# Performance work log

Hardware: AMD Instinct MI355X
Metric: run time of the kernel (lower is better)

Reference implementation:

```python
import jax, jax.numpy as jnp
import numpy as np

N, H, C, G = 50000, 16, 8, 128   # nodes, heads, per-head channels, graphs
F_IN, NUM_CLASSES = 128, 2
E = 800000
HC = H * C
NEG_SLOPE = 0.2
BN_EPS = 1e-5


def setup_inputs() -> dict:
    key = jax.random.key(0)
    ks = jax.random.split(key, 32)
    s = 0.1
    p = lambda k, shape: (jax.random.normal(k, shape, jnp.float32) * s)
    inp = {
        "x": jax.random.normal(ks[0], (N, F_IN), jnp.float32),
        "edge_index": jax.random.randint(ks[1], (2, E), 0, N, dtype=jnp.int32),
        "batch": jnp.sort(jax.random.randint(ks[2], (N,), 0, G, dtype=jnp.int32)),
        # GAT layer 1 (in=F_IN)
        "W1": p(ks[3], (F_IN, HC)), "b1": p(ks[4], (HC,)),
        "asrc1": p(ks[5], (H, C)), "adst1": p(ks[6], (H, C)),
        "g1": 1.0 + p(ks[7], (HC,)), "beta1": p(ks[8], (HC,)),
        # GAT layer 2 (in=HC)
        "W2": p(ks[9], (HC, HC)), "b2": p(ks[10], (HC,)),
        "asrc2": p(ks[11], (H, C)), "adst2": p(ks[12], (H, C)),
        "g2": 1.0 + p(ks[13], (HC,)), "beta2": p(ks[14], (HC,)),
        # GAT layer 3
        "W3": p(ks[15], (HC, HC)), "b3": p(ks[16], (HC,)),
        "asrc3": p(ks[17], (H, C)), "adst3": p(ks[18], (H, C)),
        "g3": 1.0 + p(ks[19], (HC,)), "beta3": p(ks[20], (HC,)),
        # final linear + bn4
        "Wl": p(ks[21], (2 * HC, NUM_CLASSES)), "bl": p(ks[22], (NUM_CLASSES,)),
        "g4": 1.0 + p(ks[23], (NUM_CLASSES,)), "beta4": p(ks[24], (NUM_CLASSES,)),
    }
    return inp


def _gat(x, src, dst, W, b, asrc, adst):
    # x: [N, F_in] -> h: [N, H, C]
    h = (x @ W).reshape(N, H, C)
    a_s = jnp.einsum("nhc,hc->nh", h, asrc)  # [N,H]
    a_d = jnp.einsum("nhc,hc->nh", h, adst)
    e = jax.nn.leaky_relu(a_s[src] + a_d[dst], NEG_SLOPE)  # [E',H]
    # per-destination softmax (every node has a self loop -> segments non-empty)
    e_max = jax.ops.segment_max(e, dst, num_segments=N)
    ex = jnp.exp(e - e_max[dst])
    denom = jax.ops.segment_sum(ex, dst, num_segments=N)
    alpha = ex / (denom[dst] + 1e-16)  # [E',H]
    out = jax.ops.segment_sum(h[src] * alpha[:, :, None], dst, num_segments=N)
    return out.reshape(N, HC) + b


def _bn(x, g, beta):
    mu = jnp.mean(x, axis=0)
    var = jnp.mean((x - mu) ** 2, axis=0)  # biased, training-mode BN
    return (x - mu) * jax.lax.rsqrt(var + BN_EPS) * g + beta


def reference(x, edge_index, batch,
              W1, b1, asrc1, adst1, g1, beta1,
              W2, b2, asrc2, adst2, g2, beta2,
              W3, b3, asrc3, adst3, g3, beta3,
              Wl, bl, g4, beta4):
    # add self loops once (add_self_loops=True in every GATConv)
    loop = jnp.arange(N, dtype=edge_index.dtype)
    src = jnp.concatenate([edge_index[0], loop])
    dst = jnp.concatenate([edge_index[1], loop])

    h = jax.nn.relu(_bn(_gat(x, src, dst, W1, b1, asrc1, adst1), g1, beta1))
    h = jax.nn.relu(_bn(_gat(h, src, dst, W2, b2, asrc2, adst2), g2, beta2))
    h = jax.nn.relu(_bn(_gat(h, src, dst, W3, b3, asrc3, adst3), g3, beta3))

    pooled_sum = jax.ops.segment_sum(h, batch, num_segments=G)        # [G,HC]
    cnt = jax.ops.segment_sum(jnp.ones((N,), h.dtype), batch, num_segments=G)
    pooled_mean = pooled_sum / jnp.maximum(cnt, 1.0)[:, None]
    z = jnp.concatenate([pooled_mean, pooled_sum], axis=1)            # [G,2*HC]
    z = z @ Wl + bl
    return _bn(z, g4, beta4)
```

## Files before the change

### kernel.cpp

```cpp
#include <hip/hip_runtime.h>

#define NN 50000
#define NHEADS 16
#define NGRAPH 128
#define NEDGE 800000
#define NEP (NEDGE + NN)

#define EPB 2048
#define NBLK 416
#define NBUK 391
#define CASTB 3125
#define WTB 192

typedef float4 f4;
typedef __attribute__((ext_vector_type(4))) float f32x4;
typedef __attribute__((ext_vector_type(8))) short s8;

__device__ inline unsigned short f2b(float f) {
  union { float f; unsigned u; } v; v.f = f;
  unsigned r = v.u + 0x7FFFu + ((v.u >> 16) & 1u);
  return (unsigned short)(r >> 16);
}
__device__ inline float b2f(unsigned u16) {
  union { unsigned u; float f; } v; v.u = u16 << 16;
  return v.f;
}


__global__ __launch_bounds__(256) void k_bhist(const int* __restrict__ ei, int* __restrict__ cntmat) {
  __shared__ int hist[NBUK];
  int t = threadIdx.x, b = blockIdx.x;
  for (int k = t; k < NBUK; k += 256) hist[k] = 0;
  __syncthreads();
  int i0 = b * EPB;
  int i1 = i0 + EPB < NEP ? i0 + EPB : NEP;
  for (int i = i0 + t; i < i1; i += 256) {
    int d = (i < NEDGE) ? ei[NEDGE + i] : (i - NEDGE);
    atomicAdd(&hist[d >> 7], 1);
  }
  __syncthreads();
  for (int k = t; k < NBUK; k += 256) cntmat[b * NBUK + k] = hist[k];
}

__global__ __launch_bounds__(512) void k_bscan(int* __restrict__ cntmat, int* __restrict__ btotal) {
  __shared__ int buf[512];
  int t = threadIdx.x, k = blockIdx.x;
  int v = (t < NBLK) ? cntmat[t * NBUK + k] : 0;
  buf[t] = v;
  __syncthreads();
  for (int off = 1; off < 512; off <<= 1) {
    int y = (t >= off) ? buf[t - off] : 0;
    __syncthreads();
    buf[t] += y;
    __syncthreads();
  }
  if (t < NBLK) cntmat[t * NBUK + k] = buf[t] - v;
  if (t == 511) btotal[k] = buf[511];
}

__global__ __launch_bounds__(512) void k_bbase(const int* __restrict__ btotal, int* __restrict__ bbase) {
  __shared__ int buf[512];
  int t = threadIdx.x;
  int v = (t < NBUK) ? btotal[t] : 0;
  buf[t] = v;
  __syncthreads();
  for (int off = 1; off < 512; off <<= 1) {
    int y = (t >= off) ? buf[t - off] : 0;
    __syncthreads();
    buf[t] += y;
    __syncthreads();
  }
  if (t < NBUK) bbase[t] = buf[t] - v;
  if (t == 511) bbase[NBUK] = buf[511];
}

__global__ __launch_bounds__(256) void k_bscatter(const int* __restrict__ ei, const int* __restrict__ cntmat,
                                                  const int* __restrict__ bbase, unsigned* __restrict__ pairs) {
  __shared__ int cur[NBUK];
  int t = threadIdx.x, b = blockIdx.x;
  for (int k = t; k < NBUK; k += 256) cur[k] = bbase[k] + cntmat[b * NBUK + k];
  __syncthreads();
  int i0 = b * EPB;
  int i1 = i0 + EPB < NEP ? i0 + EPB : NEP;
  for (int i = i0 + t; i < i1; i += 256) {
    int s, d;
    if (i < NEDGE) { s = ei[i]; d = ei[NEDGE + i]; }
    else { s = d = i - NEDGE; }
    int pos = atomicAdd(&cur[d >> 7], 1);
    pairs[pos] = ((unsigned)(d & 127) << 16) | (unsigned)s;
  }
}

__global__ __launch_bounds__(256) void k_bfinal(const unsigned* __restrict__ pairs, const int* __restrict__ bbase,
                                                int* __restrict__ row_off, int* __restrict__ colp) {
  __shared__ int cnt[128];
  __shared__ int buf[128];
  __shared__ int cur[128];
  int t = threadIdx.x, k = blockIdx.x;
  int n0 = k << 7;
  if (t < 128) cnt[t] = 0;
  __syncthreads();
  int p0 = bbase[k], p1 = bbase[k + 1];
  for (int i = p0 + t; i < p1; i += 256) atomicAdd(&cnt[pairs[i] >> 16], 1);
  __syncthreads();
  if (t < 128) buf[t] = cnt[t];
  __syncthreads();
  for (int off = 1; off < 128; off <<= 1) {
    int y = (t < 128 && t >= off) ? buf[t - off] : 0;
    __syncthreads();
    if (t < 128) buf[t] += y;
    __syncthreads();
  }
  if (t < 128) {
    int excl = buf[t] - cnt[t];
    cur[t] = p0 + excl;
    if (n0 + t < NN) row_off[n0 + t] = p0 + excl;
  }
  if (k == NBUK - 1 && t == 0) row_off[NN] = p1;
  __syncthreads();
  for (int i = p0 + t; i < p1; i += 256) {
    unsigned r = pairs[i];
    int pos = atomicAdd(&cur[r >> 16], 1);
    colp[pos] = (int)(r & 0xffffu);
  }
}


__global__ __launch_bounds__(256) void k_prep(const float* __restrict__ X, unsigned short* __restrict__ Xb,
                                              const float* __restrict__ W0, const float* __restrict__ W1, const float* __restrict__ W2,
                                              unsigned short* __restrict__ T0, unsigned short* __restrict__ T1, unsigned short* __restrict__ T2,
                                              const int* __restrict__ batch, int* __restrict__ gstart) {
  int b = blockIdx.x, t = threadIdx.x;
  if (b < CASTB) {
    int i = b * 256 + t;
    const f4* X4 = (const f4*)X;
    f4 a = X4[2 * i], c = X4[2 * i + 1];
    uint4 o;
    o.x = (unsigned)f2b(a.x) | ((unsigned)f2b(a.y) << 16);
    o.y = (unsigned)f2b(a.z) | ((unsigned)f2b(a.w) << 16);
    o.z = (unsigned)f2b(c.x) | ((unsigned)f2b(c.y) << 16);
    o.w = (unsigned)f2b(c.z) | ((unsigned)f2b(c.w) << 16);
    ((uint4*)Xb)[i] = o;
  } else if (b < CASTB + WTB) {
    int idx = (b - CASTB) * 256 + t;
    int L = idx >> 14, r = idx & 16383;
    int n = r >> 7, kk = r & 127;
    const float* W = (L == 0) ? W0 : (L == 1) ? W1 : W2;
    unsigned short* T = (L == 0) ? T0 : (L == 1) ? T1 : T2;
    T[n * 128 + kk] = f2b(W[kk * 128 + n]);
  } else {
    int g = t;
    if (g > NGRAPH) return;
    int lo = 0, hi = NN;
    while (lo < hi) { int mid = (lo + hi) >> 1; if (batch[mid] < g) lo = mid + 1; else hi = mid; }
    gstart[g] = lo;
  }
}


__global__ __launch_bounds__(256) void k_gemm(const unsigned short* __restrict__ Xb, const unsigned short* __restrict__ Wt,
                                              unsigned short* __restrict__ Hb) {
  int w = threadIdx.x >> 6, l = threadIdx.x & 63;
  int r0 = blockIdx.x * 128 + w * 32;
  int lr = l & 15, lg = l >> 4;
  f32x4 acc[2][8];
#pragma unroll
  for (int m = 0; m < 2; ++m)
#pragma unroll
    for (int n = 0; n < 8; ++n) acc[m][n] = (f32x4){0.f, 0.f, 0.f, 0.f};

#pragma unroll
  for (int ks = 0; ks < 4; ++ks) {
    int koff = ks * 32 + lg * 8;
    s8 a[2];
#pragma unroll
    for (int m = 0; m < 2; ++m) {
      int row = r0 + m * 16 + lr;
      row = (row < NN) ? row : (NN - 1);
      a[m] = *(const s8*)(Xb + (size_t)row * 128 + koff);
    }
    s8 b[8];
#pragma unroll
    for (int n = 0; n < 8; ++n)
      b[n] = *(const s8*)(Wt + (size_t)(n * 16 + lr) * 128 + koff);
#pragma unroll
    for (int m = 0; m < 2; ++m)
#pragma unroll
      for (int n = 0; n < 8; ++n)
        acc[m][n] = __builtin_amdgcn_mfma_f32_16x16x32_bf16(a[m], b[n], acc[m][n], 0, 0, 0);
  }

#pragma unroll
  for (int m = 0; m < 2; ++m) {
    int rowb = r0 + m * 16 + lg * 4;
#pragma unroll
    for (int n = 0; n < 8; ++n) {
      int colb = n * 16 + lr;
#pragma unroll
      for (int reg = 0; reg < 4; ++reg) {
        int row = rowb + reg;
        if (row < NN) Hb[(size_t)row * 128 + colb] = f2b(acc[m][n][reg]);
      }
    }
  }
}


__global__ __launch_bounds__(256) void k_coef(const unsigned short* __restrict__ Hb, const float* __restrict__ asrc,
                                              const float* __restrict__ adst, unsigned short* __restrict__ Asb, float* __restrict__ Ad) {
  int idx = blockIdx.x * 256 + threadIdx.x;
  if (idx >= NN * NHEADS) return;
  int n = idx >> 4, hd = idx & 15;
  uint4 hv = *(const uint4*)(Hb + (size_t)n * 128 + hd * 8);
  float h0 = b2f(hv.x & 0xffff), h1 = b2f(hv.x >> 16);
  float h2 = b2f(hv.y & 0xffff), h3 = b2f(hv.y >> 16);
  float h4 = b2f(hv.z & 0xffff), h5 = b2f(hv.z >> 16);
  float h6 = b2f(hv.w & 0xffff), h7 = b2f(hv.w >> 16);
  const f4* s4 = (const f4*)(asrc + hd * 8);
  const f4* d4 = (const f4*)(adst + hd * 8);
  f4 sa = s4[0], sb = s4[1], da = d4[0], db = d4[1];
  float as_v = h0 * sa.x + h1 * sa.y + h2 * sa.z + h3 * sa.w + h4 * sb.x + h5 * sb.y + h6 * sb.z + h7 * sb.w;
  float ad_v = h0 * da.x + h1 * da.y + h2 * da.z + h3 * da.w + h4 * db.x + h5 * db.y + h6 * db.z + h7 * db.w;
  Asb[idx] = f2b(as_v);
  Ad[idx] = ad_v;
}


__global__ __launch_bounds__(256) void k_agg(const unsigned short* __restrict__ Hb, const unsigned short* __restrict__ Asb,
                                             const float* __restrict__ Ad,
                                             const int* __restrict__ row_off, const int* __restrict__ col,
                                             unsigned short* __restrict__ Vb) {
  int node = blockIdx.x * 8 + (threadIdx.x >> 5);
  int l = threadIdx.x & 31;
  int h = l & 15, par = l >> 4;
  int e0 = row_off[node], e1 = row_off[node + 1];
  float adh = Ad[node * 16 + h];
  float den = 0.f;
  float acc[8] = {0.f, 0.f, 0.f, 0.f, 0.f, 0.f, 0.f, 0.f};
  int j = e0 + par;
  for (; j + 14 < e1; j += 16) {
    int s[8];
#pragma unroll
    for (int q = 0; q < 8; ++q) s[q] = col[j + 2 * q];
    float a[8];
#pragma unroll
    for (int q = 0; q < 8; ++q) a[q] = b2f(Asb[s[q] * 16 + h]);
    uint4 p[8];
#pragma unroll
    for (int q = 0; q < 8; ++q) p[q] = *(const uint4*)(Hb + (size_t)s[q] * 128 + h * 8);
#pragma unroll
    for (int q = 0; q < 8; ++q) {
      float e = a[q] + adh;
      e = (e > 0.f) ? e : 0.2f * e;
      a[q] = __expf(e);
      den += a[q];
    }
#pragma unroll
    for (int q = 0; q < 8; ++q) {
      acc[0] += a[q] * b2f(p[q].x & 0xffff); acc[1] += a[q] * b2f(p[q].x >> 16);
      acc[2] += a[q] * b2f(p[q].y & 0xffff); acc[3] += a[q] * b2f(p[q].y >> 16);
      acc[4] += a[q] * b2f(p[q].z & 0xffff); acc[5] += a[q] * b2f(p[q].z >> 16);
      acc[6] += a[q] * b2f(p[q].w & 0xffff); acc[7] += a[q] * b2f(p[q].w >> 16);
    }
  }
  for (; j + 6 < e1; j += 8) {
    int s[4];
#pragma unroll
    for (int q = 0; q < 4; ++q) s[q] = col[j + 2 * q];
    float a[4];
#pragma unroll
    for (int q = 0; q < 4; ++q) a[q] = b2f(Asb[s[q] * 16 + h]);
    uint4 p[4];
#pragma unroll
    for (int q = 0; q < 4; ++q) p[q] = *(const uint4*)(Hb + (size_t)s[q] * 128 + h * 8);
#pragma unroll
    for (int q = 0; q < 4; ++q) {
      float e = a[q] + adh;
      e = (e > 0.f) ? e : 0.2f * e;
      a[q] = __expf(e);
      den += a[q];
    }
#pragma unroll
    for (int q = 0; q < 4; ++q) {
      acc[0] += a[q] * b2f(p[q].x & 0xffff); acc[1] += a[q] * b2f(p[q].x >> 16);
      acc[2] += a[q] * b2f(p[q].y & 0xffff); acc[3] += a[q] * b2f(p[q].y >> 16);
      acc[4] += a[q] * b2f(p[q].z & 0xffff); acc[5] += a[q] * b2f(p[q].z >> 16);
      acc[6] += a[q] * b2f(p[q].w & 0xffff); acc[7] += a[q] * b2f(p[q].w >> 16);
    }
  }
  for (; j < e1; j += 2) {
    int s0 = col[j];
    float a0 = b2f(Asb[s0 * 16 + h]) + adh;
    uint4 p0 = *(const uint4*)(Hb + (size_t)s0 * 128 + h * 8);
    a0 = (a0 > 0.f) ? a0 : 0.2f * a0;
    float x0 = __expf(a0);
    den += x0;
    acc[0] += x0 * b2f(p0.x & 0xffff);
    acc[1] += x0 * b2f(p0.x >> 16);
    acc[2] += x0 * b2f(p0.y & 0xffff);
    acc[3] += x0 * b2f(p0.y >> 16);
    acc[4] += x0 * b2f(p0.z & 0xffff);
    acc[5] += x0 * b2f(p0.z >> 16);
    acc[6] += x0 * b2f(p0.w & 0xffff);
    acc[7] += x0 * b2f(p0.w >> 16);
  }
  den += __shfl_xor(den, 16);
#pragma unroll
  for (int k = 0; k < 8; ++k) acc[k] += __shfl_xor(acc[k], 16);
  if (par == 0) {
    float inv = 1.f / (den + 1e-16f);
    uint4 o;
    o.x = (unsigned)f2b(acc[0] * inv) | ((unsigned)f2b(acc[1] * inv) << 16);
    o.y = (unsigned)f2b(acc[2] * inv) | ((unsigned)f2b(acc[3] * inv) << 16);
    o.z = (unsigned)f2b(acc[4] * inv) | ((unsigned)f2b(acc[5] * inv) << 16);
    o.w = (unsigned)f2b(acc[6] * inv) | ((unsigned)f2b(acc[7] * inv) << 16);
    *(uint4*)(Vb + (size_t)node * 128 + h * 8) = o;
  }
}


#define BN_CHUNK 391

__global__ __launch_bounds__(256) void k_bnreduce(const unsigned short* __restrict__ Vb, float* __restrict__ partS, float* __restrict__ partQ) {
  int t = threadIdx.x;
  int c4 = t & 31, rs = t >> 5;
  int r0 = blockIdx.x * BN_CHUNK + rs;
  int rend = blockIdx.x * BN_CHUNK + BN_CHUNK;
  if (rend > NN) rend = NN;
  float s0 = 0.f, s1 = 0.f, s2 = 0.f, s3 = 0.f;
  float q0 = 0.f, q1 = 0.f, q2 = 0.f, q3 = 0.f;
  for (int r = r0; r < rend; r += 8) {
    uint2 p = *(const uint2*)(Vb + (size_t)r * 128 + c4 * 4);
    float v0 = b2f(p.x & 0xffff), v1 = b2f(p.x >> 16);
    float v2 = b2f(p.y & 0xffff), v3 = b2f(p.y >> 16);
    s0 += v0; s1 += v1; s2 += v2; s3 += v3;
    q0 += v0 * v0; q1 += v1 * v1; q2 += v2 * v2; q3 += v3 * v3;
  }
  __shared__ float sm[8][32][8];
  sm[rs][c4][0] = s0; sm[rs][c4][1] = s1; sm[rs][c4][2] = s2; sm[rs][c4][3] = s3;
  sm[rs][c4][4] = q0; sm[rs][c4][5] = q1; sm[rs][c4][6] = q2; sm[rs][c4][7] = q3;
  __syncthreads();
  if (t < 32) {
#pragma unroll
    for (int k = 0; k < 4; ++k) {
      float S = 0.f, Q = 0.f;
#pragma unroll
      for (int r = 0; r < 8; ++r) { S += sm[r][t][k]; Q += sm[r][t][4 + k]; }
      partS[blockIdx.x * 128 + t * 4 + k] = S;
      partQ[blockIdx.x * 128 + t * 4 + k] = Q;
    }
  }
}

__global__ __launch_bounds__(512) void k_bnfin(const float* __restrict__ partS, const float* __restrict__ partQ,
                                               const float* __restrict__ gam, const float* __restrict__ bet,
                                               float* __restrict__ sc) {
  int t = threadIdx.x;
  int c = t & 127, q = (t >> 7) & 1, hf = t >> 8;
  const float* src = q ? partQ : partS;
  float s = 0.f;
#pragma unroll 8
  for (int i = hf * 64; i < hf * 64 + 64; ++i) s += src[i * 128 + c];
  __shared__ float sm[512];
  sm[t] = s;
  __syncthreads();
  if (t < 128) {
    float S = sm[t] + sm[t + 256];
    float Q = sm[t + 128] + sm[t + 384];
    float mean = S * (1.f / NN);
    float var = fmaxf(Q * (1.f / NN) - mean * mean, 0.f);
    float sg = gam[t] * rsqrtf(var + 1e-5f);
    sc[t] = sg;
    sc[128 + t] = bet[t] - mean * sg;
  }
}

__global__ __launch_bounds__(256) void k_bnapply(const unsigned short* __restrict__ Vb, unsigned short* __restrict__ Xb,
                                                 const float* __restrict__ sc) {
  int idx = blockIdx.x * 256 + threadIdx.x;
  int c4 = idx & 31;
  uint2 p = ((const uint2*)Vb)[idx];
  f4 s = ((const f4*)sc)[c4], sh = ((const f4*)sc)[32 + c4];
  float v0 = fmaxf(b2f(p.x & 0xffff) * s.x + sh.x, 0.f);
  float v1 = fmaxf(b2f(p.x >> 16)    * s.y + sh.y, 0.f);
  float v2 = fmaxf(b2f(p.y & 0xffff) * s.z + sh.z, 0.f);
  float v3 = fmaxf(b2f(p.y >> 16)    * s.w + sh.w, 0.f);
  uint2 o;
  o.x = (unsigned)f2b(v0) | ((unsigned)f2b(v1) << 16);
  o.y = (unsigned)f2b(v2) | ((unsigned)f2b(v3) << 16);
  ((uint2*)Xb)[idx] = o;
}


__global__ __launch_bounds__(256) void k_pool(const unsigned short* __restrict__ Vb, const int* __restrict__ gstart,
                                              float* __restrict__ pooled) {
  int g = blockIdx.x >> 2, chunk = blockIdx.x & 3;
  int t = threadIdx.x;
  int c4 = t & 31, rs = t >> 5;
  int r0 = gstart[g], r1 = gstart[g + 1];
  float s0 = 0.f, s1 = 0.f, s2 = 0.f, s3 = 0.f;
  for (int r = r0 + chunk + 4 * rs; r < r1; r += 32) {
    uint2 p = *(const uint2*)(Vb + (size_t)r * 128 + c4 * 4);
    s0 += b2f(p.x & 0xffff); s1 += b2f(p.x >> 16);
    s2 += b2f(p.y & 0xffff); s3 += b2f(p.y >> 16);
  }
  __shared__ float sm[8][32][4];
  sm[rs][c4][0] = s0; sm[rs][c4][1] = s1; sm[rs][c4][2] = s2; sm[rs][c4][3] = s3;
  __syncthreads();
  if (t < 32) {
#pragma unroll
    for (int k = 0; k < 4; ++k) {
      float S = 0.f;
#pragma unroll
      for (int r = 0; r < 8; ++r) S += sm[r][t][k];
      atomicAdd(&pooled[g * 128 + t * 4 + k], S);
    }
  }
}

__global__ __launch_bounds__(256) void k_final(const float* __restrict__ pooled, const int* __restrict__ gstart,
                                               const float* __restrict__ Wl, const float* __restrict__ bl,
                                               const float* __restrict__ g4, const float* __restrict__ b4,
                                               float* __restrict__ out) {
  int t = threadIdx.x;
  int g = t >> 1, cls = t & 1;
  float cnt = fmaxf((float)(gstart[g + 1] - gstart[g]), 1.f);
  float inv = 1.f / cnt;
  float z = bl[cls];
  for (int f = 0; f < 128; ++f) {
    float ps = pooled[g * 128 + f];
    z += ps * inv * Wl[f * 2 + cls] + ps * Wl[(128 + f) * 2 + cls];
  }
  __shared__ float zs[256];
  __shared__ float st[4];
  zs[t] = z;
  __syncthreads();
  if (t < 2) {
    float s = 0.f, s2 = 0.f;
    for (int gg = 0; gg < 128; ++gg) { float v = zs[gg * 2 + t]; s += v; s2 += v * v; }
    float mean = s * (1.f / 128.f);
    float var = s2 * (1.f / 128.f) - mean * mean;
    var = fmaxf(var, 0.f);
    float sc = g4[t] * rsqrtf(var + 1e-5f);
    st[t] = sc; st[2 + t] = b4[t] - mean * sc;
  }
  __syncthreads();
  out[t] = zs[t] * st[cls] + st[2 + cls];
}


extern "C" void kernel_launch(void* const* d_in, const int* in_sizes, int n_in,
                              void* d_out, int out_size, void* d_ws, size_t ws_size,
                              hipStream_t stream) {
  const float* x     = (const float*)d_in[0];
  const int*   ei    = (const int*)d_in[1];
  const int*   batch = (const int*)d_in[2];
  const float* W[3]    = {(const float*)d_in[3],  (const float*)d_in[9],  (const float*)d_in[15]};
  const float* asrc[3] = {(const float*)d_in[5],  (const float*)d_in[11], (const float*)d_in[17]};
  const float* adst[3] = {(const float*)d_in[6],  (const float*)d_in[12], (const float*)d_in[18]};
  const float* gam[3]  = {(const float*)d_in[7],  (const float*)d_in[13], (const float*)d_in[19]};
  const float* bet[3]  = {(const float*)d_in[8],  (const float*)d_in[14], (const float*)d_in[20]};
  const float* Wl    = (const float*)d_in[21];
  const float* bl    = (const float*)d_in[22];
  const float* g4    = (const float*)d_in[23];
  const float* beta4 = (const float*)d_in[24];

  char* ws = (char*)d_ws;
  size_t off = 0;
  auto alloc = [&](size_t bytes) -> void* {
    void* p = (void*)(ws + off);
    off += (bytes + 255) & ~(size_t)255;
    return p;
  };

  int* row_off  = (int*)alloc((size_t)(NN + 1) * 4);
  int* col      = (int*)alloc((size_t)NEP * 4);
  int* cntmat   = (int*)alloc((size_t)NBLK * NBUK * 4);
  int* btotal   = (int*)alloc((size_t)NBUK * 4);
  int* bbase    = (int*)alloc((size_t)(NBUK + 1) * 4);
  unsigned* pairs = (unsigned*)alloc((size_t)NEP * 4);
  unsigned short* Xb = (unsigned short*)alloc((size_t)NN * 128 * 2);
  unsigned short* Hb = (unsigned short*)alloc((size_t)NN * 128 * 2);
  unsigned short* Vb = (unsigned short*)alloc((size_t)NN * 128 * 2);
  unsigned short* Asb = (unsigned short*)alloc((size_t)NN * 16 * 2);
  float* Ad     = (float*)alloc((size_t)NN * 16 * 4);
  unsigned short* Wt0 = (unsigned short*)alloc(16384 * 2);
  unsigned short* Wt1 = (unsigned short*)alloc(16384 * 2);
  unsigned short* Wt2 = (unsigned short*)alloc(16384 * 2);
  const unsigned short* Wt[3] = {Wt0, Wt1, Wt2};
  float* partS  = (float*)alloc(128 * 128 * 4);
  float* partQ  = (float*)alloc(128 * 128 * 4);
  float* bn_sc  = (float*)alloc(256 * 4);
  float* pooled = (float*)alloc((size_t)NGRAPH * 128 * 4);
  int* gstart   = (int*)alloc((size_t)(NGRAPH + 1) * 4);

  k_bhist<<<NBLK, 256, 0, stream>>>(ei, cntmat);
  k_bscan<<<NBUK, 512, 0, stream>>>(cntmat, btotal);
  k_bbase<<<1, 512, 0, stream>>>(btotal, bbase);
  k_bscatter<<<NBLK, 256, 0, stream>>>(ei, cntmat, bbase, pairs);
  k_bfinal<<<NBUK, 256, 0, stream>>>(pairs, bbase, row_off, col);

  k_prep<<<CASTB + WTB + 1, 256, 0, stream>>>(x, Xb, W[0], W[1], W[2], Wt0, Wt1, Wt2, batch, gstart);

  hipMemsetAsync(pooled, 0, (size_t)NGRAPH * 128 * 4, stream);

  for (int L = 0; L < 3; ++L) {
    k_gemm<<<(NN + 127) / 128, 256, 0, stream>>>(Xb, Wt[L], Hb);
    k_coef<<<(NN * 16) / 256, 256, 0, stream>>>(Hb, asrc[L], adst[L], Asb, Ad);
    k_agg<<<NN / 8, 256, 0, stream>>>(Hb, Asb, Ad, row_off, col, Vb);
    k_bnreduce<<<128, 256, 0, stream>>>(Vb, partS, partQ);
    k_bnfin<<<1, 512, 0, stream>>>(partS, partQ, gam[L], bet[L], bn_sc);
    k_bnapply<<<(NN * 32) / 256, 256, 0, stream>>>(Vb, Xb, bn_sc);
  }

  k_pool<<<NGRAPH * 4, 256, 0, stream>>>(Xb, gstart, pooled);
  k_final<<<1, 256, 0, stream>>>(pooled, gstart, Wl, bl, g4, beta4, (float*)d_out);
}
```

Baseline: 311.1 us.

## Fuse BN apply and ReLU into next GEMM's A-load and into pooling

Removes the standalone BN-apply kernel. The scale/shift plus ReLU now runs while the next layer's GEMM loads its A operand from Vb, and while pooling reads the final layer. This saves one full read and write of the node feature matrix per layer and one launch per layer. It also adds cheaper bf16 unpack helpers (masking instead of shifting for the high half) and an occupancy hint of 4 on k_agg. The cost is extra ALU work inside the GEMM load path.

```diff
diff --git a/kernel.cpp b/kernel.cpp
--- a/kernel.cpp
+++ b/kernel.cpp
@@ -23,6 +23,14 @@
 }
 __device__ inline float b2f(unsigned u16) {
   union { unsigned u; float f; } v; v.u = u16 << 16;
+  return v.f;
+}
+__device__ inline float blo(unsigned u) {
+  union { unsigned u; float f; } v; v.u = u << 16;
+  return v.f;
+}
+__device__ inline float bhi(unsigned u) {
+  union { unsigned u; float f; } v; v.u = u & 0xffff0000u;
   return v.f;
 }
 
@@ -158,8 +166,9 @@
 }
 
 
-__global__ __launch_bounds__(256) void k_gemm(const unsigned short* __restrict__ Xb, const unsigned short* __restrict__ Wt,
-                                              unsigned short* __restrict__ Hb) {
+template<int FUSE>
+__global__ __launch_bounds__(256) void k_gemm_t(const unsigned short* __restrict__ A, const unsigned short* __restrict__ Wt,
+                                                const float* __restrict__ sc, unsigned short* __restrict__ Hb) {
   int w = threadIdx.x >> 6, l = threadIdx.x & 63;
   int r0 = blockIdx.x * 128 + w * 32;
   int lr = l & 15, lg = l >> 4;
@@ -173,11 +182,36 @@
   for (int ks = 0; ks < 4; ++ks) {
     int koff = ks * 32 + lg * 8;
     s8 a[2];
-#pragma unroll
-    for (int m = 0; m < 2; ++m) {
-      int row = r0 + m * 16 + lr;
-      row = (row < NN) ? row : (NN - 1);
-      a[m] = *(const s8*)(Xb + (size_t)row * 128 + koff);
+    if constexpr (FUSE) {
+      f4 s0 = *(const f4*)(sc + koff),       s1 = *(const f4*)(sc + koff + 4);
+      f4 h0 = *(const f4*)(sc + 128 + koff), h1 = *(const f4*)(sc + 128 + koff + 4);
+#pragma unroll
+      for (int m = 0; m < 2; ++m) {
+        int row = r0 + m * 16 + lr;
+        row = (row < NN) ? row : (NN - 1);
+        uint4 raw = *(const uint4*)(A + (size_t)row * 128 + koff);
+        float v0 = fmaxf(blo(raw.x) * s0.x + h0.x, 0.f);
+        float v1 = fmaxf(bhi(raw.x) * s0.y + h0.y, 0.f);
+        float v2 = fmaxf(blo(raw.y) * s0.z + h0.z, 0.f);
+        float v3 = fmaxf(bhi(raw.y) * s0.w + h0.w, 0.f);
+        float v4 = fmaxf(blo(raw.z) * s1.x + h1.x, 0.f);
+        float v5 = fmaxf(bhi(raw.z) * s1.y + h1.y, 0.f);
+        float v6 = fmaxf(blo(raw.w) * s1.z + h1.z, 0.f);
+        float v7 = fmaxf(bhi(raw.w) * s1.w + h1.w, 0.f);
+        union { s8 v; uint4 u; } pk;
+        pk.u.x = (unsigned)f2b(v0) | ((unsigned)f2b(v1) << 16);
+        pk.u.y = (unsigned)f2b(v2) | ((unsigned)f2b(v3) << 16);
+        pk.u.z = (unsigned)f2b(v4) | ((unsigned)f2b(v5) << 16);
+        pk.u.w = (unsigned)f2b(v6) | ((unsigned)f2b(v7) << 16);
+        a[m] = pk.v;
+      }
+    } else {
+#pragma unroll
+      for (int m = 0; m < 2; ++m) {
+        int row = r0 + m * 16 + lr;
+        row = (row < NN) ? row : (NN - 1);
+        a[m] = *(const s8*)(A + (size_t)row * 128 + koff);
+      }
     }
     s8 b[8];
 #pragma unroll
@@ -212,10 +246,10 @@
   if (idx >= NN * NHEADS) return;
   int n = idx >> 4, hd = idx & 15;
   uint4 hv = *(const uint4*)(Hb + (size_t)n * 128 + hd * 8);
-  float h0 = b2f(hv.x & 0xffff), h1 = b2f(hv.x >> 16);
-  float h2 = b2f(hv.y & 0xffff), h3 = b2f(hv.y >> 16);
-  float h4 = b2f(hv.z & 0xffff), h5 = b2f(hv.z >> 16);
-  float h6 = b2f(hv.w & 0xffff), h7 = b2f(hv.w >> 16);
+  float h0 = blo(hv.x), h1 = bhi(hv.x);
+  float h2 = blo(hv.y), h3 = bhi(hv.y);
+  float h4 = blo(hv.z), h5 = bhi(hv.z);
+  float h6 = blo(hv.w), h7 = bhi(hv.w);
   const f4* s4 = (const f4*)(asrc + hd * 8);
   const f4* d4 = (const f4*)(adst + hd * 8);
   f4 sa = s4[0], sb = s4[1], da = d4[0], db = d4[1];
@@ -226,10 +260,10 @@
 }
 
 
-__global__ __launch_bounds__(256) void k_agg(const unsigned short* __restrict__ Hb, const unsigned short* __restrict__ Asb,
-                                             const float* __restrict__ Ad,
-                                             const int* __restrict__ row_off, const int* __restrict__ col,
-                                             unsigned short* __restrict__ Vb) {
+__global__ __launch_bounds__(256, 4) void k_agg(const unsigned short* __restrict__ Hb, const unsigned short* __restrict__ Asb,
+                                                const float* __restrict__ Ad,
+                                                const int* __restrict__ row_off, const int* __restrict__ col,
+                                                unsigned short* __restrict__ Vb) {
   int node = blockIdx.x * 8 + (threadIdx.x >> 5);
   int l = threadIdx.x & 31;
   int h = l & 15, par = l >> 4;
@@ -257,10 +291,10 @@
     }
 #pragma unroll
     for (int q = 0; q < 8; ++q) {
-      acc[0] += a[q] * b2f(p[q].x & 0xffff); acc[1] += a[q] * b2f(p[q].x >> 16);
-      acc[2] += a[q] * b2f(p[q].y & 0xffff); acc[3] += a[q] * b2f(p[q].y >> 16);
-      acc[4] += a[q] * b2f(p[q].z & 0xffff); acc[5] += a[q] * b2f(p[q].z >> 16);
-      acc[6] += a[q] * b2f(p[q].w & 0xffff); acc[7] += a[q] * b2f(p[q].w >> 16);
+      acc[0] += a[q] * blo(p[q].x); acc[1] += a[q] * bhi(p[q].x);
+      acc[2] += a[q] * blo(p[q].y); acc[3] += a[q] * bhi(p[q].y);
+      acc[4] += a[q] * blo(p[q].z); acc[5] += a[q] * bhi(p[q].z);
+      acc[6] += a[q] * blo(p[q].w); acc[7] += a[q] * bhi(p[q].w);
     }
   }
   for (; j + 6 < e1; j += 8) {
@@ -282,10 +316,10 @@
     }
 #pragma unroll
     for (int q = 0; q < 4; ++q) {
-      acc[0] += a[q] * b2f(p[q].x & 0xffff); acc[1] += a[q] * b2f(p[q].x >> 16);
-      acc[2] += a[q] * b2f(p[q].y & 0xffff); acc[3] += a[q] * b2f(p[q].y >> 16);
-      acc[4] += a[q] * b2f(p[q].z & 0xffff); acc[5] += a[q] * b2f(p[q].z >> 16);
-      acc[6] += a[q] * b2f(p[q].w & 0xffff); acc[7] += a[q] * b2f(p[q].w >> 16);
+      acc[0] += a[q] * blo(p[q].x); acc[1] += a[q] * bhi(p[q].x);
+      acc[2] += a[q] * blo(p[q].y); acc[3] += a[q] * bhi(p[q].y);
+      acc[4] += a[q] * blo(p[q].z); acc[5] += a[q] * bhi(p[q].z);
+      acc[6] += a[q] * blo(p[q].w); acc[7] += a[q] * bhi(p[q].w);
     }
   }
   for (; j < e1; j += 2) {
@@ -295,14 +329,10 @@
     a0 = (a0 > 0.f) ? a0 : 0.2f * a0;
     float x0 = __expf(a0);
     den += x0;
-    acc[0] += x0 * b2f(p0.x & 0xffff);
-    acc[1] += x0 * b2f(p0.x >> 16);
-    acc[2] += x0 * b2f(p0.y & 0xffff);
-    acc[3] += x0 * b2f(p0.y >> 16);
-    acc[4] += x0 * b2f(p0.z & 0xffff);
-    acc[5] += x0 * b2f(p0.z >> 16);
-    acc[6] += x0 * b2f(p0.w & 0xffff);
-    acc[7] += x0 * b2f(p0.w >> 16);
+    acc[0] += x0 * blo(p0.x); acc[1] += x0 * bhi(p0.x);
+    acc[2] += x0 * blo(p0.y); acc[3] += x0 * bhi(p0.y);
+    acc[4] += x0 * blo(p0.z); acc[5] += x0 * bhi(p0.z);
+    acc[6] += x0 * blo(p0.w); acc[7] += x0 * bhi(p0.w);
   }
   den += __shfl_xor(den, 16);
 #pragma unroll
@@ -331,8 +361,8 @@
   float q0 = 0.f, q1 = 0.f, q2 = 0.f, q3 = 0.f;
   for (int r = r0; r < rend; r += 8) {
     uint2 p = *(const uint2*)(Vb + (size_t)r * 128 + c4 * 4);
-    float v0 = b2f(p.x & 0xffff), v1 = b2f(p.x >> 16);
-    float v2 = b2f(p.y & 0xffff), v3 = b2f(p.y >> 16);
+    float v0 = blo(p.x), v1 = bhi(p.x);
+    float v2 = blo(p.y), v3 = bhi(p.y);
     s0 += v0; s1 += v1; s2 += v2; s3 += v3;
     q0 += v0 * v0; q1 += v1 * v1; q2 += v2 * v2; q3 += v3 * v3;
   }
@@ -375,34 +405,21 @@
   }
 }
 
-__global__ __launch_bounds__(256) void k_bnapply(const unsigned short* __restrict__ Vb, unsigned short* __restrict__ Xb,
-                                                 const float* __restrict__ sc) {
-  int idx = blockIdx.x * 256 + threadIdx.x;
-  int c4 = idx & 31;
-  uint2 p = ((const uint2*)Vb)[idx];
-  f4 s = ((const f4*)sc)[c4], sh = ((const f4*)sc)[32 + c4];
-  float v0 = fmaxf(b2f(p.x & 0xffff) * s.x + sh.x, 0.f);
-  float v1 = fmaxf(b2f(p.x >> 16)    * s.y + sh.y, 0.f);
-  float v2 = fmaxf(b2f(p.y & 0xffff) * s.z + sh.z, 0.f);
-  float v3 = fmaxf(b2f(p.y >> 16)    * s.w + sh.w, 0.f);
-  uint2 o;
-  o.x = (unsigned)f2b(v0) | ((unsigned)f2b(v1) << 16);
-  o.y = (unsigned)f2b(v2) | ((unsigned)f2b(v3) << 16);
-  ((uint2*)Xb)[idx] = o;
-}
-
-
-__global__ __launch_bounds__(256) void k_pool(const unsigned short* __restrict__ Vb, const int* __restrict__ gstart,
-                                              float* __restrict__ pooled) {
+
+__global__ __launch_bounds__(256) void k_pool(const unsigned short* __restrict__ Vb, const float* __restrict__ sc,
+                                              const int* __restrict__ gstart, float* __restrict__ pooled) {
   int g = blockIdx.x >> 2, chunk = blockIdx.x & 3;
   int t = threadIdx.x;
   int c4 = t & 31, rs = t >> 5;
+  f4 s = ((const f4*)sc)[c4], sh = ((const f4*)sc)[32 + c4];
   int r0 = gstart[g], r1 = gstart[g + 1];
   float s0 = 0.f, s1 = 0.f, s2 = 0.f, s3 = 0.f;
   for (int r = r0 + chunk + 4 * rs; r < r1; r += 32) {
     uint2 p = *(const uint2*)(Vb + (size_t)r * 128 + c4 * 4);
-    s0 += b2f(p.x & 0xffff); s1 += b2f(p.x >> 16);
-    s2 += b2f(p.y & 0xffff); s3 += b2f(p.y >> 16);
+    s0 += fmaxf(blo(p.x) * s.x + sh.x, 0.f);
+    s1 += fmaxf(bhi(p.x) * s.y + sh.y, 0.f);
+    s2 += fmaxf(blo(p.y) * s.z + sh.z, 0.f);
+    s3 += fmaxf(bhi(p.y) * s.w + sh.w, 0.f);
   }
   __shared__ float sm[8][32][4];
   sm[rs][c4][0] = s0; sm[rs][c4][1] = s1; sm[rs][c4][2] = s2; sm[rs][c4][3] = s3;
@@ -505,14 +522,16 @@
   hipMemsetAsync(pooled, 0, (size_t)NGRAPH * 128 * 4, stream);
 
   for (int L = 0; L < 3; ++L) {
-    k_gemm<<<(NN + 127) / 128, 256, 0, stream>>>(Xb, Wt[L], Hb);
+    if (L == 0)
+      k_gemm_t<0><<<(NN + 127) / 128, 256, 0, stream>>>(Xb, Wt[L], nullptr, Hb);
+    else
+      k_gemm_t<1><<<(NN + 127) / 128, 256, 0, stream>>>(Vb, Wt[L], bn_sc, Hb);
     k_coef<<<(NN * 16) / 256, 256, 0, stream>>>(Hb, asrc[L], adst[L], Asb, Ad);
     k_agg<<<NN / 8, 256, 0, stream>>>(Hb, Asb, Ad, row_off, col, Vb);
     k_bnreduce<<<128, 256, 0, stream>>>(Vb, partS, partQ);
     k_bnfin<<<1, 512, 0, stream>>>(partS, partQ, gam[L], bet[L], bn_sc);
-    k_bnapply<<<(NN * 32) / 256, 256, 0, stream>>>(Vb, Xb, bn_sc);
-  }
-
-  k_pool<<<NGRAPH * 4, 256, 0, stream>>>(Xb, gstart, pooled);
+  }
+
+  k_pool<<<NGRAPH * 4, 256, 0, stream>>>(Vb, bn_sc, gstart, pooled);
   k_final<<<1, 256, 0, stream>>>(pooled, gstart, Wl, bl, g4, beta4, (float*)d_out);
 }
```

New measurement: 291.2 us. 1.07x faster.
